# Kernel optimization log

Hardware: AMD Instinct MI355X
Metric: run time of the kernel (lower is better)

The kernel has to match this reference:

```python
import jax, jax.numpy as jnp
import numpy as np


def get_rel_pos(q_size, k_size, rel_pos):
    # table length == 2*max(q,k)-1, so no interpolation branch is needed.
    # relative coords: i - j + (k_size - 1) (q_size == k_size here)
    coords = jnp.arange(q_size)[:, None] - jnp.arange(k_size)[None, :] + (k_size - 1)
    return rel_pos[coords]  # (q_size, k_size, head_dim)


def setup_inputs() -> dict:
    key = jax.random.key(0)
    ks = jax.random.split(key, 11)
    B, H, W, C = 4, 32, 32, 768
    nH, d = 12, 64
    L = 2 * H - 1
    s = 0.02
    return {
        "x": jax.random.normal(ks[0], (B, H, W, C), jnp.float32),
        "Wq": jax.random.normal(ks[1], (nH, d, C), jnp.float32) * s,
        "Wk": jax.random.normal(ks[2], (nH, d, C), jnp.float32) * s,
        "Wv": jax.random.normal(ks[3], (nH, d, C), jnp.float32) * s,
        "bq": jax.random.normal(ks[4], (nH, d), jnp.float32) * s,
        "bk": jax.random.normal(ks[5], (nH, d), jnp.float32) * s,
        "bv": jax.random.normal(ks[6], (nH, d), jnp.float32) * s,
        "rel_pos_h": jax.random.normal(ks[7], (L, d), jnp.float32) * s,
        "rel_pos_w": jax.random.normal(ks[8], (L, d), jnp.float32) * s,
        "proj_w": jax.random.normal(ks[9], (C, C), jnp.float32) * s,
        "proj_b": jax.random.normal(ks[10], (C,), jnp.float32) * s,
    }


def reference(x, Wq, Wk, Wv, bq, bk, bv, rel_pos_h, rel_pos_w, proj_w, proj_b):
    B, H, W, C = x.shape
    nH, d, _ = Wq.shape
    scale = d ** -0.5
    S = H * W

    # Per-head 1x1-conv QKV projection (split-head loop in the original ==
    # one batched einsum over the head axis; same math).
    q = jnp.einsum('bhwc,ndc->bnhwd', x, Wq) + bq[None, :, None, None, :]
    k = jnp.einsum('bhwc,ndc->bnhwd', x, Wk) + bk[None, :, None, None, :]
    v = jnp.einsum('bhwc,ndc->bnhwd', x, Wv) + bv[None, :, None, None, :]

    qf = q.reshape(B, nH, S, d)
    kf = k.reshape(B, nH, S, d)
    vf = v.reshape(B, nH, S, d)

    # (q * scale) @ k^T -> (B, nH, S, S)
    attn = jnp.einsum('bnqd,bnkd->bnqk', qf * scale, kf)

    # Decomposed relative position bias
    Rh = get_rel_pos(H, H, rel_pos_h)  # (H, H, d)
    Rw = get_rel_pos(W, W, rel_pos_w)  # (W, W, d)
    rel_h = jnp.einsum('bnhwd,hkd->bnhwk', q, Rh)  # (B, nH, H, W, k_h)
    rel_w = jnp.einsum('bnhwd,wkd->bnhwk', q, Rw)  # (B, nH, H, W, k_w)
    attn = (attn.reshape(B, nH, H, W, H, W)
            + rel_h[:, :, :, :, :, None]
            + rel_w[:, :, :, :, None, :]).reshape(B, nH, S, S)

    attn = jax.nn.softmax(attn, axis=-1)
    out = jnp.einsum('bnqk,bnkd->bnqd', attn, vf)  # (B, nH, S, d)
    # concat heads: (B, nH, H, W, d) -> (B, H, W, nH*d)
    out = out.reshape(B, nH, H, W, d).transpose(0, 2, 3, 1, 4).reshape(B, H, W, nH * d)
    # output projection (1x1 conv == linear)
    return out @ proj_w.T + proj_b
```

## Files before the change

kernel.cpp:

```cpp
#include <hip/hip_runtime.h>
#include <hip/hip_bf16.h>
#include <math.h>

typedef float4 f4;
typedef __attribute__((ext_vector_type(8))) short bf16x8;
typedef __attribute__((ext_vector_type(4))) float f32x4;
typedef __attribute__((ext_vector_type(16))) float f32x16;

#define CD   768
#define SEQ  1024
#define NHD  12
#define DH   64

__device__ __forceinline__ ushort f2bf(float x) {
    union { __hip_bfloat16 h; ushort u; } v;
    v.h = __float2bfloat16(x);
    return v.u;
}
__device__ __forceinline__ unsigned pk2bf(float a, float b) {
    union { __hip_bfloat162 h; unsigned u; } v;
    v.h = __float22bfloat162_rn(make_float2(a, b));
    return v.u;
}
__device__ __forceinline__ bf16x8 mk_bf16x8(unsigned a, unsigned b, unsigned c, unsigned d) {
    union { unsigned u[4]; bf16x8 v; } r;
    r.u[0] = a; r.u[1] = b; r.u[2] = c; r.u[3] = d;
    return r.v;
}
__device__ __forceinline__ void gload_lds16(const ushort* g, ushort* l) {
    __builtin_amdgcn_global_load_lds((const __attribute__((address_space(1))) void*)g,
                                     (__attribute__((address_space(3))) void*)l, 16, 0, 0);
}

__global__ __launch_bounds__(256) void cvt_bf16_k(
    const float* __restrict__ x, const float* __restrict__ Wq,
    const float* __restrict__ Wk, const float* __restrict__ Wv,
    const float* __restrict__ pw, ushort* __restrict__ dst)
{
    const int idx = blockIdx.x * 256 + threadIdx.x;
    if (idx >= 1376256) return;
    const int e = idx << 2;
    if (e < 4915200) {
        const float* src; int off;
        if      (e < 3145728) { src = x;  off = e; }
        else if (e < 3735552) { src = Wq; off = e - 3145728; }
        else if (e < 4325376) { src = Wk; off = e - 3735552; }
        else                  { src = Wv; off = e - 4325376; }
        const f4 v = *(const f4*)(src + off);
        uint2 o;
        o.x = pk2bf(v.x, v.y);
        o.y = pk2bf(v.z, v.w);
        *(uint2*)(dst + e) = o;
    } else {
        const int off = e - 4915200;
        const int n = off / CD, k = off - n * CD;
        const f4 v = *(const f4*)(pw + off);
        uint2 o;
        o.x = pk2bf(v.x, v.y);
        o.y = pk2bf(v.z, v.w);
        *(uint2*)(dst + 4915200 + ((size_t)(k >> 6) * CD + n) * 64 + (k & 63)) = o;
    }
}

__global__ __launch_bounds__(256, 2) void qkv_mfma(
    const ushort* __restrict__ xbf,
    const ushort* __restrict__ wq, const ushort* __restrict__ wk, const ushort* __restrict__ wv,
    const float* __restrict__ bq, const float* __restrict__ bk, const float* __restrict__ bv,
    ushort* __restrict__ qbf, ushort* __restrict__ kbf, ushort* __restrict__ vbfT)
{
    __shared__ __align__(16) ushort Sq[28672];

    const int t = threadIdx.x;
    const int w = t >> 6, l = t & 63;
    const int lr = l & 15, lg = l >> 4;
    const int n0 = blockIdx.x * 96;
    const int m0 = blockIdx.y << 7;
    const int sel  = n0 / CD;
    const int nloc = n0 % CD;
    const ushort* Wb  = (sel == 0) ? wq : ((sel == 1) ? wk : wv);
    const float* bias = (sel == 0) ? bq : ((sel == 1) ? bk : bv);

    const int srow = (w << 3) + (l >> 3);
    const int scol = (l & 7) << 3;
    const ushort* Agl = xbf + (size_t)(m0 + srow) * CD + scol;
    const ushort* Bgl = Wb + (size_t)(nloc + srow) * CD + scol;

    f32x4 acc[4][3];
    #pragma unroll
    for (int mi = 0; mi < 4; ++mi)
        #pragma unroll
        for (int ni = 0; ni < 3; ++ni) acc[mi][ni] = (f32x4){0.f, 0.f, 0.f, 0.f};

    const int mb = (w >> 1) << 6;
    const int nb = (w & 1) * 48;

    #pragma unroll
    for (int i = 0; i < 4; ++i)
        gload_lds16(Agl + (size_t)(i << 5) * CD, &Sq[(i << 11) + (w << 9)]);
    #pragma unroll
    for (int i = 0; i < 3; ++i)
        gload_lds16(Bgl + (size_t)(i << 5) * CD, &Sq[8192 + (i << 11) + (w << 9)]);
    __syncthreads();

    for (int kt = 0; kt < 12; ++kt) {
        const int cb = (kt & 1) * 14336;
        if (kt < 11) {
            const int nbuf = ((kt + 1) & 1) * 14336;
            const int kc = (kt + 1) << 6;
            #pragma unroll
            for (int i = 0; i < 4; ++i)
                gload_lds16(Agl + (size_t)(i << 5) * CD + kc, &Sq[nbuf + (i << 11) + (w << 9)]);
            #pragma unroll
            for (int i = 0; i < 3; ++i)
                gload_lds16(Bgl + (size_t)(i << 5) * CD + kc, &Sq[nbuf + 8192 + (i << 11) + (w << 9)]);
        }
        #pragma unroll
        for (int kk = 0; kk < 2; ++kk) {
            bf16x8 af[4], bf[3];
            #pragma unroll
            for (int mi = 0; mi < 4; ++mi)
                af[mi] = *(const bf16x8*)&Sq[cb + (mb + (mi << 4) + lr) * 64 + (kk << 5) + (lg << 3)];
            #pragma unroll
            for (int ni = 0; ni < 3; ++ni)
                bf[ni] = *(const bf16x8*)&Sq[cb + 8192 + (nb + (ni << 4) + lr) * 64 + (kk << 5) + (lg << 3)];
            #pragma unroll
            for (int mi = 0; mi < 4; ++mi)
                #pragma unroll
                for (int ni = 0; ni < 3; ++ni)
                    acc[mi][ni] = __builtin_amdgcn_mfma_f32_16x16x32_bf16(af[mi], bf[ni], acc[mi][ni], 0, 0, 0);
        }
        __syncthreads();
    }

    ushort* Ep = Sq + w * 3072;

    float bl[3];
    #pragma unroll
    for (int ni = 0; ni < 3; ++ni) bl[ni] = bias[nloc + nb + (ni << 4) + lr];

    if (sel < 2) {
        #pragma unroll
        for (int mi = 0; mi < 4; ++mi)
            #pragma unroll
            for (int ni = 0; ni < 3; ++ni)
                #pragma unroll
                for (int reg = 0; reg < 4; ++reg)
                    Ep[((mi << 4) + (lg << 2) + reg) * 48 + (ni << 4) + lr] =
                        f2bf(acc[mi][ni][reg] + bl[ni]);
    } else {
        #pragma unroll
        for (int mi = 0; mi < 4; ++mi)
            #pragma unroll
            for (int ni = 0; ni < 3; ++ni)
                #pragma unroll
                for (int reg = 0; reg < 4; ++reg)
                    Ep[((ni << 4) + lr) * 64 +
                       ((mi >> 1) << 5) + (lg << 3) + ((mi & 1) << 2) + reg] =
                        f2bf(acc[mi][ni][reg] + bl[ni]);
    }
    __syncthreads();

    const int bi  = m0 >> 10;
    const int si0 = (m0 & 1023) + mb;
    if (sel < 2) {
        ushort* dbf = (sel == 0) ? qbf : kbf;
        #pragma unroll
        for (int i = 0; i < 6; ++i) {
            const int c0   = i << 3;
            const int head = (nloc + nb + c0) >> 6;
            const int dd0  = (nloc + nb + c0) & 63;
            const int bn   = bi * NHD + head;
            *(bf16x8*)(dbf + (((size_t)bn << 10) + si0 + l) * 64 + dd0) =
                *(const bf16x8*)(Ep + l * 48 + c0);
        }
    } else {
        #pragma unroll
        for (int i = 0; i < 6; ++i) {
            const int idx = (i << 6) + l;
            const int r   = idx >> 3, ch = idx & 7;
            const int head = (nloc + nb + r) >> 6;
            const int d    = (nloc + nb + r) & 63;
            const int bn   = bi * NHD + head;
            *(bf16x8*)(vbfT + (((size_t)(bn * DH + d)) << 10) + si0 + (ch << 3)) =
                *(const bf16x8*)(Ep + r * 64 + (ch << 3));
        }
    }
}

__global__ __launch_bounds__(256, 3) void attn_mfma(
    const ushort* __restrict__ qbf, const ushort* __restrict__ kbf,
    const ushort* __restrict__ vbfT,
    const float* __restrict__ rph, const float* __restrict__ rpw,
    ushort* __restrict__ abf2)
{
    __shared__ __align__(16) ushort KV[2][8192];
    __shared__ __align__(16) float rhs_[2048];

    const int t  = threadIdx.x;
    const int l  = t & 63, w = t >> 6;
    const int lr = l & 15, lg = l >> 4;
    const int qt = blockIdx.x, bn = blockIdx.y;
    const int q0 = qt << 6;

    {
        const int p   = w >> 1;
        const int sub = w & 1;
        const int h   = (qt << 1) + p;
        const int q5  = l & 31, g = l >> 5;

        const ushort* qp = qbf + (((size_t)bn << 10) + (h << 5) + q5) * 64 + (g << 3);
        bf16x8 qf[4];
        #pragma unroll
        for (int c = 0; c < 4; ++c) qf[c] = *(const bf16x8*)(qp + (c << 4));

        float* PwF = (float*)&KV[0][0] + p * 2112;

        if (sub == 0) {
            f32x16 acch;
            #pragma unroll
            for (int i = 0; i < 16; ++i) acch[i] = 0.f;
            {
                const float* rp = rph + (size_t)(h + 31 - q5) * 64 + (g << 3);
                #pragma unroll
                for (int c = 0; c < 4; ++c) {
                    const f4 v0 = *(const f4*)(rp + (c << 4));
                    const f4 v1 = *(const f4*)(rp + (c << 4) + 4);
                    union { unsigned u[4]; bf16x8 v; } u;
                    u.u[0] = pk2bf(v0.x, v0.y); u.u[1] = pk2bf(v0.z, v0.w);
                    u.u[2] = pk2bf(v1.x, v1.y); u.u[3] = pk2bf(v1.z, v1.w);
                    acch = __builtin_amdgcn_mfma_f32_32x32x16_bf16(u.v, qf[c], acch, 0, 0, 0);
                }
            }
            #pragma unroll
            for (int r = 0; r < 16; r += 2) {
                const int k2 = (r & 3) + ((r >> 2) << 3) + (g << 2);
                *(float2*)&rhs_[((k2 >> 1) << 7) + (((p << 5) + q5) << 1)] =
                    make_float2(acch[r], acch[r + 1]);
            }
            f32x16 accw;
            #pragma unroll
            for (int i = 0; i < 16; ++i) accw[i] = 0.f;
            {
                const float* rp = rpw + (size_t)q5 * 64 + (g << 3);
                #pragma unroll
                for (int c = 0; c < 4; ++c) {
                    const f4 v0 = *(const f4*)(rp + (c << 4));
                    const f4 v1 = *(const f4*)(rp + (c << 4) + 4);
                    union { unsigned u[4]; bf16x8 v; } u;
                    u.u[0] = pk2bf(v0.x, v0.y); u.u[1] = pk2bf(v0.z, v0.w);
                    u.u[2] = pk2bf(v1.x, v1.y); u.u[3] = pk2bf(v1.z, v1.w);
                    accw = __builtin_amdgcn_mfma_f32_32x32x16_bf16(u.v, qf[c], accw, 0, 0, 0);
                }
            }
            #pragma unroll
            for (int r = 0; r < 16; ++r) {
                const int row = (r & 3) + ((r >> 2) << 3) + (g << 2);
                PwF[row * 33 + q5] = accw[r];
            }
        } else {
            f32x16 accw;
            #pragma unroll
            for (int i = 0; i < 16; ++i) accw[i] = 0.f;
            {
                const bool ok = (32 + q5) < 63;
                const float* rp = rpw + (size_t)(32 + q5) * 64 + (g << 3);
                #pragma unroll
                for (int c = 0; c < 4; ++c) {
                    union { unsigned u[4]; bf16x8 v; } u;
                    if (ok) {
                        const f4 v0 = *(const f4*)(rp + (c << 4));
                        const f4 v1 = *(const f4*)(rp + (c << 4) + 4);
                        u.u[0] = pk2bf(v0.x, v0.y); u.u[1] = pk2bf(v0.z, v0.w);
                        u.u[2] = pk2bf(v1.x, v1.y); u.u[3] = pk2bf(v1.z, v1.w);
                    } else {
                        u.u[0] = 0u; u.u[1] = 0u; u.u[2] = 0u; u.u[3] = 0u;
                    }
                    accw = __builtin_amdgcn_mfma_f32_32x32x16_bf16(u.v, qf[c], accw, 0, 0, 0);
                }
            }
            #pragma unroll
            for (int r = 0; r < 16; ++r) {
                const int row = (r & 3) + ((r >> 2) << 3) + (g << 2) + 32;
                PwF[row * 33 + q5] = accw[r];
            }
        }
    }
    __syncthreads();

    float rw8[8];
    {
        const int p   = w >> 1;
        const int q5w = ((w & 1) << 4) + lr;
        const float* PwF = (float*)&KV[0][0] + p * 2112;
        #pragma unroll
        for (int b = 0; b < 2; ++b)
            #pragma unroll
            for (int reg = 0; reg < 4; ++reg) {
                const int k2 = (b << 4) + (lg << 2) + reg;
                rw8[(b << 2) + reg] = PwF[(q5w + 31 - k2) * 33 + q5w];
            }
    }
    __syncthreads();

    const ushort* qp = qbf + (((size_t)bn << 10) + q0 + w * 16 + lr) * DH + lg * 8;
    const bf16x8 qa0 = *(const bf16x8*)qp;
    const bf16x8 qa1 = *(const bf16x8*)(qp + 32);

    const int rhbase = (w * 16 + lr) << 1;

    const int i0   = w << 1;
    const int rsub = l >> 3;
    const int coff = ((l & 7) ^ rsub) << 3;
    const size_t kbase = ((size_t)bn << 16);
    const ushort* kp0 = kbf + kbase + (size_t)((i0 << 3) + rsub) * 64 + coff;
    const ushort* kp1 = kp0 + 512;
    const ushort* vp0 = vbfT + kbase + ((size_t)((i0 << 3) + rsub) << 10) + coff;
    const ushort* vp1 = vp0 + 8192;
    const int lds0 = i0 << 9;

    f32x4 oc[4];
    #pragma unroll
    for (int nf = 0; nf < 4; ++nf) oc[nf] = (f32x4){0.f, 0.f, 0.f, 0.f};
    f32x4 sumc = (f32x4){0.f, 0.f, 0.f, 0.f};
    bf16x8 ones;
    #pragma unroll
    for (int i = 0; i < 8; ++i) ones[i] = (short)0x3F80;

    const int s0c = lg ^ (lr & 7);

    gload_lds16(kp0, &KV[0][lds0]);
    gload_lds16(kp1, &KV[0][lds0 + 512]);
    gload_lds16(vp0, &KV[0][4096 + lds0]);
    gload_lds16(vp1, &KV[0][4096 + lds0 + 512]);
    __syncthreads();

    for (int kt = 0; kt < 16; ++kt) {
        const int cur = kt & 1;
        if (kt < 15) {
            ushort* nb_ = &KV[cur ^ 1][0];
            gload_lds16(kp0 + ((kt + 1) << 12), nb_ + lds0);
            gload_lds16(kp1 + ((kt + 1) << 12), nb_ + lds0 + 512);
            gload_lds16(vp0 + ((kt + 1) << 6), nb_ + 4096 + lds0);
            gload_lds16(vp1 + ((kt + 1) << 6), nb_ + 4096 + lds0 + 512);
        }
        const ushort* Kl = &KV[cur][0];
        const ushort* Vt = &KV[cur][4096];
        const float2 rh = *(const float2*)&rhs_[(kt << 7) + rhbase];

        f32x4 sc[4];
        #pragma unroll
        for (int f = 0; f < 4; ++f) {
            f32x4 c = (f32x4){0.f, 0.f, 0.f, 0.f};
            const int rb = (f * 16 + lr) * 64;
            const bf16x8 kb0 = *(const bf16x8*)&Kl[rb + (s0c << 3)];
            const bf16x8 kb1 = *(const bf16x8*)&Kl[rb + ((s0c ^ 4) << 3)];
            c = __builtin_amdgcn_mfma_f32_16x16x32_bf16(kb0, qa0, c, 0, 0, 0);
            c = __builtin_amdgcn_mfma_f32_16x16x32_bf16(kb1, qa1, c, 0, 0, 0);
            sc[f] = c;
        }

        unsigned ua[4], ub[4];
        #pragma unroll
        for (int f = 0; f < 4; ++f) {
            const float rhv = (f & 2) ? rh.y : rh.x;
            const int rb8 = (f & 1) << 2;
            const float e0 = __expf(fmaf(sc[f][0], 0.125f, rhv + rw8[rb8 + 0]));
            const float e1 = __expf(fmaf(sc[f][1], 0.125f, rhv + rw8[rb8 + 1]));
            const float e2 = __expf(fmaf(sc[f][2], 0.125f, rhv + rw8[rb8 + 2]));
            const float e3 = __expf(fmaf(sc[f][3], 0.125f, rhv + rw8[rb8 + 3]));
            unsigned* du = (f & 2) ? ub : ua;
            du[((f & 1) << 1) + 0] = pk2bf(e0, e1);
            du[((f & 1) << 1) + 1] = pk2bf(e2, e3);
        }
        const bf16x8 pa0 = mk_bf16x8(ua[0], ua[1], ua[2], ua[3]);
        const bf16x8 pa1 = mk_bf16x8(ub[0], ub[1], ub[2], ub[3]);

        sumc = __builtin_amdgcn_mfma_f32_16x16x32_bf16(pa0, ones, sumc, 0, 0, 0);
        sumc = __builtin_amdgcn_mfma_f32_16x16x32_bf16(pa1, ones, sumc, 0, 0, 0);
        #pragma unroll
        for (int nf = 0; nf < 4; ++nf) {
            const int rb = (nf * 16 + lr) * 64;
            const bf16x8 vb0 = *(const bf16x8*)&Vt[rb + (s0c << 3)];
            const bf16x8 vb1 = *(const bf16x8*)&Vt[rb + ((s0c ^ 4) << 3)];
            oc[nf] = __builtin_amdgcn_mfma_f32_16x16x32_bf16(pa0, vb0, oc[nf], 0, 0, 0);
            oc[nf] = __builtin_amdgcn_mfma_f32_16x16x32_bf16(pa1, vb1, oc[nf], 0, 0, 0);
        }
        __syncthreads();
    }

    const int bi = bn / NHD, hn = bn - bi * NHD;
    #pragma unroll
    for (int reg = 0; reg < 4; ++reg) {
        const float inv = 1.f / sumc[reg];
        const int row = q0 + w * 16 + lg * 4 + reg;
        ushort* dst = abf2 + ((size_t)hn * 4096 + (bi << 10) + row) * 64 + lr;
        union { unsigned u; ushort2 s2; } a, b;
        a.u = pk2bf(oc[0][reg] * inv, oc[1][reg] * inv);
        b.u = pk2bf(oc[2][reg] * inv, oc[3][reg] * inv);
        dst[0]  = a.s2.x;
        dst[16] = a.s2.y;
        dst[32] = b.s2.x;
        dst[48] = b.s2.y;
    }
}

__global__ __launch_bounds__(256, 2) void proj_mfma(
    const ushort* __restrict__ abf2, const ushort* __restrict__ pwbf2,
    const float* __restrict__ pb, float* __restrict__ out)
{
    __shared__ __align__(16) ushort Sp[20480];

    const int t = threadIdx.x;
    const int w = t >> 6, l = t & 63;
    const int lr = l & 15, lg = l >> 4;
    const int n0 = blockIdx.x * 96;
    const int m0 = blockIdx.y << 6;

    const int srow = l >> 3;
    const int scol = (l & 7) << 3;
    const ushort* Agl = abf2 + (size_t)(m0 + (w << 4) + srow) * 64 + scol;
    const ushort* Bgl = pwbf2 + (size_t)(n0 + w * 24 + srow) * 64 + scol;

    f32x4 acc[2][3];
    #pragma unroll
    for (int mi = 0; mi < 2; ++mi)
        #pragma unroll
        for (int ni = 0; ni < 3; ++ni) acc[mi][ni] = (f32x4){0.f, 0.f, 0.f, 0.f};

    const int mb = (w >> 1) << 5;
    const int nb = (w & 1) * 48;

    #pragma unroll
    for (int i = 0; i < 2; ++i)
        gload_lds16(Agl + (i << 9), &Sp[(w << 10) + (i << 9)]);
    #pragma unroll
    for (int j = 0; j < 3; ++j)
        gload_lds16(Bgl + (j << 9), &Sp[4096 + w * 1536 + (j << 9)]);
    __syncthreads();

    for (int kt = 0; kt < 12; ++kt) {
        const int cb = (kt & 1) * 10240;
        if (kt < 11) {
            const int nbuf = ((kt + 1) & 1) * 10240;
            const size_t pA = (size_t)(kt + 1) * 262144;
            const size_t pB = (size_t)(kt + 1) * 49152;
            #pragma unroll
            for (int i = 0; i < 2; ++i)
                gload_lds16(Agl + pA + (i << 9), &Sp[nbuf + (w << 10) + (i << 9)]);
            #pragma unroll
            for (int j = 0; j < 3; ++j)
                gload_lds16(Bgl + pB + (j << 9), &Sp[nbuf + 4096 + w * 1536 + (j << 9)]);
        }
        #pragma unroll
        for (int kk = 0; kk < 2; ++kk) {
            bf16x8 af[2], bf[3];
            #pragma unroll
            for (int mi = 0; mi < 2; ++mi)
                af[mi] = *(const bf16x8*)&Sp[cb + (mb + (mi << 4) + lr) * 64 + (kk << 5) + (lg << 3)];
            #pragma unroll
            for (int ni = 0; ni < 3; ++ni)
                bf[ni] = *(const bf16x8*)&Sp[cb + 4096 + (nb + (ni << 4) + lr) * 64 + (kk << 5) + (lg << 3)];
            #pragma unroll
            for (int mi = 0; mi < 2; ++mi)
                #pragma unroll
                for (int ni = 0; ni < 3; ++ni)
                    acc[mi][ni] = __builtin_amdgcn_mfma_f32_16x16x32_bf16(af[mi], bf[ni], acc[mi][ni], 0, 0, 0);
        }
        __syncthreads();
    }

    float bl[3];
    #pragma unroll
    for (int ni = 0; ni < 3; ++ni) bl[ni] = pb[n0 + nb + (ni << 4) + lr];
    #pragma unroll
    for (int mi = 0; mi < 2; ++mi)
        #pragma unroll
        for (int ni = 0; ni < 3; ++ni)
            #pragma unroll
            for (int reg = 0; reg < 4; ++reg)
                out[(size_t)(m0 + mb + (mi << 4) + (lg << 2) + reg) * CD
                    + n0 + nb + (ni << 4) + lr] = acc[mi][ni][reg] + bl[ni];
}

extern "C" void kernel_launch(void* const* d_in, const int* in_sizes, int n_in,
                              void* d_out, int out_size, void* d_ws, size_t ws_size,
                              hipStream_t stream) {
    (void)in_sizes; (void)n_in; (void)out_size; (void)ws_size;
    const float* x   = (const float*)d_in[0];
    const float* Wq  = (const float*)d_in[1];
    const float* Wk  = (const float*)d_in[2];
    const float* Wv  = (const float*)d_in[3];
    const float* bq  = (const float*)d_in[4];
    const float* bk  = (const float*)d_in[5];
    const float* bv  = (const float*)d_in[6];
    const float* rph = (const float*)d_in[7];
    const float* rpw = (const float*)d_in[8];
    const float* pw  = (const float*)d_in[9];
    const float* pb  = (const float*)d_in[10];
    float* out = (float*)d_out;

    ushort* cvt  = (ushort*)d_ws;
    ushort* xbf  = cvt;
    ushort* wqbf = cvt + 3145728;
    ushort* wkbf = wqbf + 589824;
    ushort* wvbf = wkbf + 589824;
    ushort* pwbf = wvbf + 589824;
    ushort* qbf  = pwbf + 589824;
    ushort* kbf  = qbf  + 3145728;
    ushort* vbfT = kbf  + 3145728;
    ushort* abf2 = vbfT + 3145728;

    hipLaunchKernelGGL(cvt_bf16_k, dim3(5376), dim3(256), 0, stream,
                       x, Wq, Wk, Wv, pw, cvt);
    hipLaunchKernelGGL(qkv_mfma, dim3(24, 32), dim3(256), 0, stream,
                       xbf, wqbf, wkbf, wvbf, bq, bk, bv, qbf, kbf, vbfT);
    hipLaunchKernelGGL(attn_mfma, dim3(16, 48), dim3(256), 0, stream,
                       qbf, kbf, vbfT, rph, rpw, abf2);
    hipLaunchKernelGGL(proj_mfma, dim3(8, 64), dim3(256), 0, stream,
                       abf2, pwbf, pb, out);
}
```

Baseline: 79.61 us.

## Fuse four stages into one persistent cooperative kernel with grid syncs

Replaces the four separate launches (convert, QKV GEMM, attention, projection) with one persistent cooperative kernel. Blocks loop over tiles of each stage and meet at grid-wide barriers, which removes the gaps between kernel launches. To fit a shared LDS buffer sized for three blocks per CU, the QKV GEMM drops its double-buffered LDS prefetch and becomes single-buffered with two barriers per k-step, which exposes load latency. The host also makes several device and occupancy queries on every call, and falls back to four separate kernels if the cooperative launch fails.

```diff
diff --git a/kernel.cpp b/kernel.cpp
--- a/kernel.cpp
+++ b/kernel.cpp
@@ -1,6 +1,9 @@
 #include <hip/hip_runtime.h>
+#include <hip/hip_cooperative_groups.h>
 #include <hip/hip_bf16.h>
 #include <math.h>
+
+namespace cg = cooperative_groups;
 
 typedef float4 f4;
 typedef __attribute__((ext_vector_type(8))) short bf16x8;
@@ -32,13 +35,12 @@
                                      (__attribute__((address_space(3))) void*)l, 16, 0, 0);
 }
 
-__global__ __launch_bounds__(256) void cvt_bf16_k(
-    const float* __restrict__ x, const float* __restrict__ Wq,
+
+__device__ __forceinline__ void dev_cvt(
+    int idx, const float* __restrict__ x, const float* __restrict__ Wq,
     const float* __restrict__ Wk, const float* __restrict__ Wv,
-    const float* __restrict__ pw, ushort* __restrict__ dst)
-{
-    const int idx = blockIdx.x * 256 + threadIdx.x;
-    if (idx >= 1376256) return;
+    const float* __restrict__ pw, ushort* __restrict__ ws)
+{
     const int e = idx << 2;
     if (e < 4915200) {
         const float* src; int off;
@@ -50,7 +52,7 @@
         uint2 o;
         o.x = pk2bf(v.x, v.y);
         o.y = pk2bf(v.z, v.w);
-        *(uint2*)(dst + e) = o;
+        *(uint2*)(ws + e) = o;
     } else {
         const int off = e - 4915200;
         const int n = off / CD, k = off - n * CD;
@@ -58,26 +60,25 @@
         uint2 o;
         o.x = pk2bf(v.x, v.y);
         o.y = pk2bf(v.z, v.w);
-        *(uint2*)(dst + 4915200 + ((size_t)(k >> 6) * CD + n) * 64 + (k & 63)) = o;
-    }
-}
-
-__global__ __launch_bounds__(256, 2) void qkv_mfma(
+        *(uint2*)(ws + 4915200 + ((size_t)(k >> 6) * CD + n) * 64 + (k & 63)) = o;
+    }
+}
+
+__device__ __forceinline__ void dev_qkv(
+    int tile, ushort* Sq,
     const ushort* __restrict__ xbf,
-    const ushort* __restrict__ wq, const ushort* __restrict__ wk, const ushort* __restrict__ wv,
+    const ushort* __restrict__ wqbf, const ushort* __restrict__ wkbf, const ushort* __restrict__ wvbf,
     const float* __restrict__ bq, const float* __restrict__ bk, const float* __restrict__ bv,
     ushort* __restrict__ qbf, ushort* __restrict__ kbf, ushort* __restrict__ vbfT)
 {
-    __shared__ __align__(16) ushort Sq[28672];
-
     const int t = threadIdx.x;
     const int w = t >> 6, l = t & 63;
     const int lr = l & 15, lg = l >> 4;
-    const int n0 = blockIdx.x * 96;
-    const int m0 = blockIdx.y << 7;
+    const int n0 = (tile % 24) * 96;
+    const int m0 = (tile / 24) << 7;
     const int sel  = n0 / CD;
     const int nloc = n0 % CD;
-    const ushort* Wb  = (sel == 0) ? wq : ((sel == 1) ? wk : wv);
+    const ushort* Wb  = (sel == 0) ? wqbf : ((sel == 1) ? wkbf : wvbf);
     const float* bias = (sel == 0) ? bq : ((sel == 1) ? bk : bv);
 
     const int srow = (w << 3) + (l >> 3);
@@ -94,43 +95,33 @@
     const int mb = (w >> 1) << 6;
     const int nb = (w & 1) * 48;
 
-    #pragma unroll
-    for (int i = 0; i < 4; ++i)
-        gload_lds16(Agl + (size_t)(i << 5) * CD, &Sq[(i << 11) + (w << 9)]);
-    #pragma unroll
-    for (int i = 0; i < 3; ++i)
-        gload_lds16(Bgl + (size_t)(i << 5) * CD, &Sq[8192 + (i << 11) + (w << 9)]);
-    __syncthreads();
-
     for (int kt = 0; kt < 12; ++kt) {
-        const int cb = (kt & 1) * 14336;
-        if (kt < 11) {
-            const int nbuf = ((kt + 1) & 1) * 14336;
-            const int kc = (kt + 1) << 6;
-            #pragma unroll
-            for (int i = 0; i < 4; ++i)
-                gload_lds16(Agl + (size_t)(i << 5) * CD + kc, &Sq[nbuf + (i << 11) + (w << 9)]);
-            #pragma unroll
-            for (int i = 0; i < 3; ++i)
-                gload_lds16(Bgl + (size_t)(i << 5) * CD + kc, &Sq[nbuf + 8192 + (i << 11) + (w << 9)]);
-        }
+        const int kc = kt << 6;
+        __syncthreads();
+        #pragma unroll
+        for (int i = 0; i < 4; ++i)
+            gload_lds16(Agl + (size_t)(i << 5) * CD + kc, &Sq[(i << 11) + (w << 9)]);
+        #pragma unroll
+        for (int i = 0; i < 3; ++i)
+            gload_lds16(Bgl + (size_t)(i << 5) * CD + kc, &Sq[8192 + (i << 11) + (w << 9)]);
+        __syncthreads();
         #pragma unroll
         for (int kk = 0; kk < 2; ++kk) {
             bf16x8 af[4], bf[3];
             #pragma unroll
             for (int mi = 0; mi < 4; ++mi)
-                af[mi] = *(const bf16x8*)&Sq[cb + (mb + (mi << 4) + lr) * 64 + (kk << 5) + (lg << 3)];
+                af[mi] = *(const bf16x8*)&Sq[(mb + (mi << 4) + lr) * 64 + (kk << 5) + (lg << 3)];
             #pragma unroll
             for (int ni = 0; ni < 3; ++ni)
-                bf[ni] = *(const bf16x8*)&Sq[cb + 8192 + (nb + (ni << 4) + lr) * 64 + (kk << 5) + (lg << 3)];
+                bf[ni] = *(const bf16x8*)&Sq[8192 + (nb + (ni << 4) + lr) * 64 + (kk << 5) + (lg << 3)];
             #pragma unroll
             for (int mi = 0; mi < 4; ++mi)
                 #pragma unroll
                 for (int ni = 0; ni < 3; ++ni)
                     acc[mi][ni] = __builtin_amdgcn_mfma_f32_16x16x32_bf16(af[mi], bf[ni], acc[mi][ni], 0, 0, 0);
         }
-        __syncthreads();
-    }
+    }
+    __syncthreads();
 
     ushort* Ep = Sq + w * 3072;
 
@@ -187,20 +178,23 @@
     }
 }
 
-__global__ __launch_bounds__(256, 3) void attn_mfma(
+__device__ __forceinline__ void dev_attn(
+    int tile, ushort* SMEM,
     const ushort* __restrict__ qbf, const ushort* __restrict__ kbf,
     const ushort* __restrict__ vbfT,
     const float* __restrict__ rph, const float* __restrict__ rpw,
     ushort* __restrict__ abf2)
 {
-    __shared__ __align__(16) ushort KV[2][8192];
-    __shared__ __align__(16) float rhs_[2048];
+    ushort (*KV)[8192] = (ushort(*)[8192])SMEM;
+    float* rhs_ = (float*)(SMEM + 16384);
 
     const int t  = threadIdx.x;
     const int l  = t & 63, w = t >> 6;
     const int lr = l & 15, lg = l >> 4;
-    const int qt = blockIdx.x, bn = blockIdx.y;
+    const int qt = tile & 15, bn = tile >> 4;
     const int q0 = qt << 6;
+
+    __syncthreads();
 
     {
         const int p   = w >> 1;
@@ -404,22 +398,21 @@
     }
 }
 
-__global__ __launch_bounds__(256, 2) void proj_mfma(
-    const ushort* __restrict__ abf2, const ushort* __restrict__ pwbf2,
+__device__ __forceinline__ void dev_proj(
+    int tile, ushort* Sp,
+    const ushort* __restrict__ abf2, const ushort* __restrict__ pwbf,
     const float* __restrict__ pb, float* __restrict__ out)
 {
-    __shared__ __align__(16) ushort Sp[20480];
-
     const int t = threadIdx.x;
     const int w = t >> 6, l = t & 63;
     const int lr = l & 15, lg = l >> 4;
-    const int n0 = blockIdx.x * 96;
-    const int m0 = blockIdx.y << 6;
+    const int n0 = (tile & 7) * 96;
+    const int m0 = (tile >> 3) << 6;
 
     const int srow = l >> 3;
     const int scol = (l & 7) << 3;
     const ushort* Agl = abf2 + (size_t)(m0 + (w << 4) + srow) * 64 + scol;
-    const ushort* Bgl = pwbf2 + (size_t)(n0 + w * 24 + srow) * 64 + scol;
+    const ushort* Bgl = pwbf + (size_t)(n0 + w * 24 + srow) * 64 + scol;
 
     f32x4 acc[2][3];
     #pragma unroll
@@ -430,6 +423,7 @@
     const int mb = (w >> 1) << 5;
     const int nb = (w & 1) * 48;
 
+    __syncthreads();
     #pragma unroll
     for (int i = 0; i < 2; ++i)
         gload_lds16(Agl + (i << 9), &Sp[(w << 10) + (i << 9)]);
@@ -480,6 +474,84 @@
             for (int reg = 0; reg < 4; ++reg)
                 out[(size_t)(m0 + mb + (mi << 4) + (lg << 2) + reg) * CD
                     + n0 + nb + (ni << 4) + lr] = acc[mi][ni][reg] + bl[ni];
+}
+
+__global__ __launch_bounds__(256, 3) void mega_k(
+    const float* __restrict__ x,
+    const float* __restrict__ Wq, const float* __restrict__ Wk, const float* __restrict__ Wv,
+    const float* __restrict__ bq, const float* __restrict__ bk, const float* __restrict__ bv,
+    const float* __restrict__ rph, const float* __restrict__ rpw,
+    const float* __restrict__ pw, const float* __restrict__ pb,
+    float* __restrict__ out, ushort* __restrict__ ws)
+{
+    __shared__ __align__(16) ushort SMEM[20480];
+
+    ushort* xbf  = ws;
+    ushort* wqbf = ws + 3145728;
+    ushort* wkbf = wqbf + 589824;
+    ushort* wvbf = wkbf + 589824;
+    ushort* pwbf = wvbf + 589824;
+    ushort* qbf  = pwbf + 589824;
+    ushort* kbf  = qbf  + 3145728;
+    ushort* vbfT = kbf  + 3145728;
+    ushort* abf2 = vbfT + 3145728;
+
+    cg::grid_group grid = cg::this_grid();
+
+    for (int idx = blockIdx.x * 256 + threadIdx.x; idx < 1376256; idx += gridDim.x << 8)
+        dev_cvt(idx, x, Wq, Wk, Wv, pw, ws);
+    __threadfence();
+    grid.sync();
+
+    for (int tile = blockIdx.x; tile < 768; tile += gridDim.x)
+        dev_qkv(tile, SMEM, xbf, wqbf, wkbf, wvbf, bq, bk, bv, qbf, kbf, vbfT);
+    __threadfence();
+    grid.sync();
+
+    for (int tile = blockIdx.x; tile < 768; tile += gridDim.x)
+        dev_attn(tile, SMEM, qbf, kbf, vbfT, rph, rpw, abf2);
+    __threadfence();
+    grid.sync();
+
+    for (int tile = blockIdx.x; tile < 512; tile += gridDim.x)
+        dev_proj(tile, SMEM, abf2, pwbf, pb, out);
+}
+
+__global__ __launch_bounds__(256, 2) void cvt_k(
+    const float* __restrict__ x, const float* __restrict__ Wq,
+    const float* __restrict__ Wk, const float* __restrict__ Wv,
+    const float* __restrict__ pw, ushort* __restrict__ ws)
+{
+    const int idx = blockIdx.x * 256 + threadIdx.x;
+    if (idx < 1376256) dev_cvt(idx, x, Wq, Wk, Wv, pw, ws);
+}
+
+__global__ __launch_bounds__(256, 2) void qkv_k(
+    const ushort* __restrict__ xbf,
+    const ushort* __restrict__ wqbf, const ushort* __restrict__ wkbf, const ushort* __restrict__ wvbf,
+    const float* __restrict__ bq, const float* __restrict__ bk, const float* __restrict__ bv,
+    ushort* __restrict__ qbf, ushort* __restrict__ kbf, ushort* __restrict__ vbfT)
+{
+    __shared__ __align__(16) ushort S[14336];
+    dev_qkv(blockIdx.x, S, xbf, wqbf, wkbf, wvbf, bq, bk, bv, qbf, kbf, vbfT);
+}
+
+__global__ __launch_bounds__(256, 3) void attn_k(
+    const ushort* __restrict__ qbf, const ushort* __restrict__ kbf,
+    const ushort* __restrict__ vbfT,
+    const float* __restrict__ rph, const float* __restrict__ rpw,
+    ushort* __restrict__ abf2)
+{
+    __shared__ __align__(16) ushort S[20480];
+    dev_attn(blockIdx.x, S, qbf, kbf, vbfT, rph, rpw, abf2);
+}
+
+__global__ __launch_bounds__(256, 2) void proj_k(
+    const ushort* __restrict__ abf2, const ushort* __restrict__ pwbf,
+    const float* __restrict__ pb, float* __restrict__ out)
+{
+    __shared__ __align__(16) ushort S[20480];
+    dev_proj(blockIdx.x, S, abf2, pwbf, pb, out);
 }
 
 extern "C" void kernel_launch(void* const* d_in, const int* in_sizes, int n_in,
@@ -498,24 +570,50 @@
     const float* pw  = (const float*)d_in[9];
     const float* pb  = (const float*)d_in[10];
     float* out = (float*)d_out;
-
-    ushort* cvt  = (ushort*)d_ws;
-    ushort* xbf  = cvt;
-    ushort* wqbf = cvt + 3145728;
-    ushort* wkbf = wqbf + 589824;
-    ushort* wvbf = wkbf + 589824;
-    ushort* pwbf = wvbf + 589824;
-    ushort* qbf  = pwbf + 589824;
-    ushort* kbf  = qbf  + 3145728;
-    ushort* vbfT = kbf  + 3145728;
-    ushort* abf2 = vbfT + 3145728;
-
-    hipLaunchKernelGGL(cvt_bf16_k, dim3(5376), dim3(256), 0, stream,
-                       x, Wq, Wk, Wv, pw, cvt);
-    hipLaunchKernelGGL(qkv_mfma, dim3(24, 32), dim3(256), 0, stream,
-                       xbf, wqbf, wkbf, wvbf, bq, bk, bv, qbf, kbf, vbfT);
-    hipLaunchKernelGGL(attn_mfma, dim3(16, 48), dim3(256), 0, stream,
-                       qbf, kbf, vbfT, rph, rpw, abf2);
-    hipLaunchKernelGGL(proj_mfma, dim3(8, 64), dim3(256), 0, stream,
-                       abf2, pwbf, pb, out);
-}
+    ushort* ws = (ushort*)d_ws;
+
+    int dev = 0;
+    hipGetDevice(&dev);
+    int coop = 0;
+    hipDeviceGetAttribute(&coop, hipDeviceAttributeCooperativeLaunch, dev);
+    int ncu = 0;
+    hipDeviceGetAttribute(&ncu, hipDeviceAttributeMultiprocessorCount, dev);
+    int occ = 0;
+    hipOccupancyMaxActiveBlocksPerMultiprocessor(&occ, mega_k, 256, 0);
+
+    hipError_t st = hipErrorUnknown;
+    if (coop && ncu > 0 && occ > 0) {
+        int grid = occ * ncu;
+        if (grid > 768) grid = 768;
+        if (grid >= 192) {
+            void* args[] = {
+                (void*)&x, (void*)&Wq, (void*)&Wk, (void*)&Wv,
+                (void*)&bq, (void*)&bk, (void*)&bv,
+                (void*)&rph, (void*)&rpw, (void*)&pw, (void*)&pb,
+                (void*)&out, (void*)&ws
+            };
+            st = hipLaunchCooperativeKernel((const void*)mega_k, dim3(grid), dim3(256),
+                                            args, 0, stream);
+        }
+    }
+    if (st != hipSuccess) {
+        ushort* xbf  = ws;
+        ushort* wqbf = ws + 3145728;
+        ushort* wkbf = wqbf + 589824;
+        ushort* wvbf = wkbf + 589824;
+        ushort* pwbf = wvbf + 589824;
+        ushort* qbf  = pwbf + 589824;
+        ushort* kbf  = qbf  + 3145728;
+        ushort* vbfT = kbf  + 3145728;
+        ushort* abf2 = vbfT + 3145728;
+
+        hipLaunchKernelGGL(cvt_k, dim3(5376), dim3(256), 0, stream,
+                           x, Wq, Wk, Wv, pw, ws);
+        hipLaunchKernelGGL(qkv_k, dim3(768), dim3(256), 0, stream,
+                           xbf, wqbf, wkbf, wvbf, bq, bk, bv, qbf, kbf, vbfT);
+        hipLaunchKernelGGL(attn_k, dim3(768), dim3(256), 0, stream,
+                           qbf, kbf, vbfT, rph, rpw, abf2);
+        hipLaunchKernelGGL(proj_k, dim3(512), dim3(256), 0, stream,
+                           abf2, pwbf, pb, out);
+    }
+}
```

New measurement: 305.8 us. 3.84x slower.
